# Kernel tuning notes

Hardware: AMD Instinct MI355X
Metric: run time of the kernel (lower is better)

## Reference

```python
import jax, jax.numpy as jnp
import numpy as np

U1, U2, FEAT = 24, 48, 16
LN_EPS = 1e-3  # tf.keras LayerNormalization default


def _ln(x, gamma, beta):
    mu = jnp.mean(x, axis=-1, keepdims=True)
    var = jnp.mean(jnp.square(x - mu), axis=-1, keepdims=True)
    return (x - mu) * jax.lax.rsqrt(var + LN_EPS) * gamma + beta


def setup_inputs() -> dict:
    key = jax.random.key(0)
    ks = jax.random.split(key, 8)
    B, T = 8192, 256
    sequence = jax.random.normal(ks[0], (B, T, FEAT), dtype=jnp.float32)
    s = 0.1
    return {
        "sequence": sequence,
        "W1": jax.random.normal(ks[1], (FEAT, U1), dtype=jnp.float32) * s,
        "b1": jnp.zeros((U1,), jnp.float32),
        "Wr1": jax.random.normal(ks[2], (U1, U1), dtype=jnp.float32) * s,
        "br1": jnp.zeros((U1,), jnp.float32),
        "g1": jnp.ones((U1,), jnp.float32),
        "be1": jnp.zeros((U1,), jnp.float32),
        "W2": jax.random.normal(ks[3], (U1, U2), dtype=jnp.float32) * s,
        "b2": jnp.zeros((U2,), jnp.float32),
        "Wr2": jax.random.normal(ks[4], (U2, U2), dtype=jnp.float32) * s,
        "br2": jnp.zeros((U2,), jnp.float32),
        "g2": jnp.ones((U2,), jnp.float32),
        "be2": jnp.zeros((U2,), jnp.float32),
        "Wout": jax.random.normal(ks[5], (U2, 1), dtype=jnp.float32) * s,
        "bout": jnp.zeros((1,), jnp.float32),
    }


def reference(sequence, W1, b1, Wr1, br1, g1, be1, W2, b2, Wr2, br2, g2, be2, Wout, bout):
    B = sequence.shape[0]
    xs = jnp.swapaxes(sequence, 0, 1)  # [T, B, F]

    def step(carry, inp):
        s1, s2 = carry
        x = inp @ W1 + b1 + s1
        ns1 = jnp.tanh(x @ Wr1 + br1)
        h = _ln(ns1, g1, be1)
        y = h @ W2 + b2 + s2
        ns2 = jnp.tanh(y @ Wr2 + br2)
        return (ns1, ns2), None

    init = (jnp.zeros((B, U1), sequence.dtype), jnp.zeros((B, U2), sequence.dtype))
    (s1, s2), _ = jax.lax.scan(step, init, xs)
    last_out = _ln(s2, g2, be2)  # output of final timestep (return_sequences=False)
    return jax.nn.sigmoid(last_out @ Wout + bout)  # [B, 1]
```

## Files before the change

kernel.cpp:

```cpp
#include <hip/hip_runtime.h>

#define T_STEPS 256
#define FEAT 16
#define U1 24
#define U2 48
#define SLOTS 8

typedef short bf16x8 __attribute__((ext_vector_type(8)));
typedef float f32x4 __attribute__((ext_vector_type(4)));

__device__ __forceinline__ unsigned short f2bf(float f) {
    unsigned u = __float_as_uint(f);
    u += 0x7fffu + ((u >> 16) & 1u);
    return (unsigned short)(u >> 16);
}

#if defined(__has_builtin)
#if __has_builtin(__builtin_amdgcn_cvt_pk_bf16_f32)
#define HAVE_PKBF16 1
#endif
#if __has_builtin(__builtin_amdgcn_rcpf)
#define HAVE_RCP 1
#endif
#if __has_builtin(__builtin_amdgcn_rsqf)
#define HAVE_RSQ 1
#endif
#if __has_builtin(__builtin_amdgcn_exp2f)
#define HAVE_EXP2 1
#endif
#endif

__device__ __forceinline__ unsigned pk2(float a, float b) {
#ifdef HAVE_PKBF16
    typedef __bf16 bf2 __attribute__((ext_vector_type(2)));
    union { bf2 v; unsigned u; } cv;
    cv.v = __builtin_amdgcn_cvt_pk_bf16_f32(a, b);
    return cv.u;
#else
    return (unsigned)f2bf(a) | ((unsigned)f2bf(b) << 16);
#endif
}
__device__ __forceinline__ float bfr(float x) {
    return __uint_as_float(((unsigned)f2bf(x)) << 16);
}

__device__ __forceinline__ float hrcp(float x) {
#ifdef HAVE_RCP
    return __builtin_amdgcn_rcpf(x);
#else
    return 1.0f / x;
#endif
}
__device__ __forceinline__ float hrsq(float x) {
#ifdef HAVE_RSQ
    return __builtin_amdgcn_rsqf(x);
#else
    return rsqrtf(x);
#endif
}
__device__ __forceinline__ float hexp2(float x) {
#ifdef HAVE_EXP2
    return __builtin_amdgcn_exp2f(x);
#else
    return exp2f(x);
#endif
}
__device__ __forceinline__ float fast_tanh(float z) {
    const float e = hexp2(z * 2.8853900817779268f);
    return fmaf(-2.0f, hrcp(1.0f + e), 1.0f);
}

union FragU { bf16x8 v; unsigned u[4]; };

#define MFMA(A, B, C) __builtin_amdgcn_mfma_f32_16x16x32_bf16((A), (B), (C), 0, 0, 0)

__device__ __forceinline__ void bar_sync() {
    asm volatile("" ::: "memory");
    __builtin_amdgcn_s_waitcnt(0xC07F);
    __builtin_amdgcn_s_barrier();
    asm volatile("" ::: "memory");
}


__global__ __launch_bounds__(128) void rnn_kernel(
    const float* __restrict__ seq,
    const float* __restrict__ W1, const float* __restrict__ b1,
    const float* __restrict__ Wr1, const float* __restrict__ br1,
    const float* __restrict__ g1, const float* __restrict__ be1,
    const float* __restrict__ W2, const float* __restrict__ b2,
    const float* __restrict__ Wr2, const float* __restrict__ br2,
    const float* __restrict__ g2, const float* __restrict__ be2,
    const float* __restrict__ Wout, const float* __restrict__ bout,
    float* __restrict__ out)
{
    __shared__ __align__(16) unsigned ringN[SLOTS][64][4];
    __shared__ __align__(16) unsigned ringQ[SLOTS][64][4];

    const int tid = threadIdx.x;
    const int w = tid >> 6;
    const int lane = tid & 63;
    const int j15 = lane & 15;
    const int g = lane >> 4;
    const f32x4 z4 = {0.f, 0.f, 0.f, 0.f};

    if (w == 0) {
        bf16x8 A1[2], A2[2];
#pragma unroll
        for (int t = 0; t < 2; ++t) {
            const int m = 16 * t + j15;
            FragU f1, f2;
#pragma unroll
            for (int j = 0; j < 8; ++j) {
                const int k = 8 * g + j;
                const int u = (j < 4) ? 4 * g + j : 16 + 4 * g + (j - 4);
                float v1 = 0.f, v2 = 0.f;
                if (m < U1) {
                    if (k < FEAT) v1 = W1[k * U1 + m];
                    else if (k == FEAT) v1 = b1[m];
                    if (u < U1) v2 = Wr1[u * U1 + m];
                    else if (u == U1) v2 = br1[m];
                } else if (m == U1 && k == FEAT) {
                    v1 = 1.f;
                }
                f1.v[j] = (short)f2bf(v1);
                f2.v[j] = (short)f2bf(v2);
            }
            A1[t] = f1.v; A2[t] = f2.v;
        }
        const unsigned cdw0 = (g == 2) ? 0x00003F80u : 0u;

        const float* sp = seq + (size_t)(blockIdx.x * 16 + j15) * (T_STEPS * FEAT) + 8 * g;
        const bool ld = (lane < 32);

        f32x4 s1[2] = {z4, z4};

        auto pstep = [&](int t, const float4 ca, const float4 cb) {
            FragU inf;
            const unsigned p0 = pk2(ca.x, ca.y), p1 = pk2(ca.z, ca.w);
            const unsigned p2 = pk2(cb.x, cb.y), p3 = pk2(cb.z, cb.w);
            const bool lo = (g < 2);
            inf.u[0] = lo ? p0 : cdw0;
            inf.u[1] = lo ? p1 : 0u;
            inf.u[2] = lo ? p2 : 0u;
            inf.u[3] = lo ? p3 : 0u;

            const f32x4 x0 = MFMA(A1[0], inf.v, s1[0]);
            const f32x4 x1 = MFMA(A1[1], inf.v, s1[1]);

            FragU xf;
            xf.u[0] = pk2(x0[0], x0[1]); xf.u[1] = pk2(x0[2], x0[3]);
            xf.u[2] = pk2(x1[0], x1[1]); xf.u[3] = pk2(x1[2], x1[3]);

            const f32x4 d0 = MFMA(A2[0], xf.v, z4);
            const f32x4 d1 = MFMA(A2[1], xf.v, z4);
            float n1a[4], n1b[4], qa[4], qb[4];
#pragma unroll
            for (int r = 0; r < 4; ++r) {
                n1a[r] = fast_tanh(d0[r]); n1b[r] = fast_tanh(d1[r]);
                qa[r] = n1a[r] * n1a[r];   qb[r] = n1b[r] * n1b[r];
                s1[0][r] = n1a[r];         s1[1][r] = n1b[r];
            }
            FragU nf, qf;
            nf.u[0] = pk2(n1a[0], n1a[1]); nf.u[1] = pk2(n1a[2], n1a[3]);
            nf.u[2] = pk2(n1b[0], n1b[1]); nf.u[3] = pk2(n1b[2], n1b[3]);
            qf.u[0] = pk2(qa[0], qa[1]);   qf.u[1] = pk2(qa[2], qa[3]);
            qf.u[2] = pk2(qb[0], qb[1]);   qf.u[3] = pk2(qb[2], qb[3]);
            const int slot = t & (SLOTS - 1);
            *(uint4*)&ringN[slot][lane][0] = make_uint4(nf.u[0], nf.u[1], nf.u[2], nf.u[3]);
            *(uint4*)&ringQ[slot][lane][0] = make_uint4(qf.u[0], qf.u[1], qf.u[2], qf.u[3]);
        };

        float4 ca[4], cb[4], na[4], nb[4];
        if (ld) {
#pragma unroll
            for (int i = 0; i < 4; ++i) {
                ca[i] = *(const float4*)(sp + i * 16);
                cb[i] = *(const float4*)(sp + i * 16 + 4);
            }
        }
#pragma unroll 1
        for (int j = 0; j < 64; ++j) {
            const int jn = (j + 1 < 64) ? j + 1 : j;
            if (ld) {
#pragma unroll
                for (int i = 0; i < 4; ++i) {
                    na[i] = *(const float4*)(sp + (4 * jn + i) * 16);
                    nb[i] = *(const float4*)(sp + (4 * jn + i) * 16 + 4);
                }
            }
#pragma unroll
            for (int i = 0; i < 4; ++i) pstep(4 * j + i, ca[i], cb[i]);
            bar_sync();
#pragma unroll
            for (int i = 0; i < 4; ++i) { ca[i] = na[i]; cb[i] = nb[i]; }
        }
        bar_sync();
    } else {
        bf16x8 A3a[4], A3b3, A4[3][2];
#pragma unroll
        for (int t = 0; t < 3; ++t) {
            const int m = 16 * t + j15;
            FragU f3, f4a, f4b;
#pragma unroll
            for (int j = 0; j < 8; ++j) {
                const int u = (j < 4) ? 4 * g + j : 16 + 4 * g + (j - 4);
                f3.v[j] = (short)f2bf(u < U1 ? g1[u] * W2[u * U2 + m] : 0.f);
                f4a.v[j] = (short)f2bf(Wr2[u * U2 + m]);
                float vb = 0.f;
                if (j < 4) vb = Wr2[(32 + 4 * g + j) * U2 + m];
                else if (j == 4 && g == 0) vb = br2[m];
                f4b.v[j] = (short)f2bf(vb);
            }
            A3a[t] = f3.v; A4[t][0] = f4a.v; A4[t][1] = f4b.v;
        }
        {
            FragU fa, fb;
#pragma unroll
            for (int j = 0; j < 8; ++j) {
                const int u = (j < 4) ? 4 * g + j : 16 + 4 * g + (j - 4);
                fa.v[j] = ((j15 & 3) == 0 && u < U1) ? (short)0x3F80 : (short)0;
                fb.v[j] = ((j15 & 3) == 1 && u < U1) ? (short)0x3F80 : (short)0;
            }
            A3a[3] = fa.v; A3b3 = fb.v;
        }
        float cC[12], dC[12];
#pragma unroll
        for (int i = 0; i < 12; ++i) {
            const int m = 16 * (i >> 2) + 4 * g + (i & 3);
            float cc = 0.f, dd = b2[m];
            for (int k = 0; k < U1; ++k) {
                const float wq = bfr(g1[k] * W2[k * U2 + m]);
                cc += wq;
                dd += be1[k] * W2[k * U2 + m];
            }
            cC[i] = cc; dC[i] = dd;
        }
        f32x4 s2[3] = {z4, z4, z4};

        auto cstep = [&](int t) {
            const int slot = t & (SLOTS - 1);
            const bf16x8 hf0 = *(const bf16x8*)&ringN[slot][lane][0];
            const bf16x8 hf1 = *(const bf16x8*)&ringQ[slot][lane][0];

            f32x4 sAcc = MFMA(A3a[3], hf0, z4);
            sAcc = MFMA(A3b3, hf1, sAcc);
            const f32x4 P0 = MFMA(A3a[0], hf0, z4);
            const f32x4 P1 = MFMA(A3a[1], hf0, z4);
            const f32x4 P2 = MFMA(A3a[2], hf0, z4);

            const float mu = sAcc[0] * (1.f / U1);
            const float var = sAcc[1] * (1.f / U1) - mu * mu;
            const float rs = hrsq(var + 1e-3f);

            float y[12];
#pragma unroll
            for (int r = 0; r < 4; ++r) {
                y[r]     = fmaf(rs, fmaf(-mu, cC[r],     P0[r]), dC[r]     + s2[0][r]);
                y[4 + r] = fmaf(rs, fmaf(-mu, cC[4 + r], P1[r]), dC[4 + r] + s2[1][r]);
                y[8 + r] = fmaf(rs, fmaf(-mu, cC[8 + r], P2[r]), dC[8 + r] + s2[2][r]);
            }

            FragU yf0, yf1;
            yf0.u[0] = pk2(y[0], y[1]);  yf0.u[1] = pk2(y[2], y[3]);
            yf0.u[2] = pk2(y[4], y[5]);  yf0.u[3] = pk2(y[6], y[7]);
            yf1.u[0] = pk2(y[8], y[9]);  yf1.u[1] = pk2(y[10], y[11]);
            yf1.u[2] = (g == 0) ? 0x00003F80u : 0u;
            yf1.u[3] = 0u;

#pragma unroll
            for (int t3 = 0; t3 < 3; ++t3) {
                f32x4 e = MFMA(A4[t3][0], yf0.v, z4);
                e = MFMA(A4[t3][1], yf1.v, e);
#pragma unroll
                for (int r = 0; r < 4; ++r) s2[t3][r] = fast_tanh(e[r]);
            }
        };

        bar_sync();
#pragma unroll 1
        for (int j = 0; j < 64; ++j) {
#pragma unroll
            for (int i = 0; i < 4; ++i) cstep(4 * j + i);
            bar_sync();
        }

        float g2r[12], be2r[12], wor[12];
#pragma unroll
        for (int r = 0; r < 12; ++r) {
            const int n = 16 * (r >> 2) + 4 * g + (r & 3);
            g2r[r] = g2[n]; be2r[r] = be2[n]; wor[r] = Wout[n];
        }
        float sm = 0.f, sq = 0.f;
#pragma unroll
        for (int tt = 0; tt < 3; ++tt)
#pragma unroll
            for (int r = 0; r < 4; ++r) { const float v = s2[tt][r]; sm += v; sq += v * v; }
        sm += __shfl_xor(sm, 16, 64); sq += __shfl_xor(sq, 16, 64);
        sm += __shfl_xor(sm, 32, 64); sq += __shfl_xor(sq, 32, 64);
        const float mu = sm * (1.f / U2);
        const float var = sq * (1.f / U2) - mu * mu;
        const float rs = hrsq(var + 1e-3f);
        float p = 0.f;
#pragma unroll
        for (int tt = 0; tt < 3; ++tt)
#pragma unroll
            for (int r = 0; r < 4; ++r)
                p += ((s2[tt][r] - mu) * rs * g2r[4 * tt + r] + be2r[4 * tt + r]) * wor[4 * tt + r];
        p += __shfl_xor(p, 16, 64);
        p += __shfl_xor(p, 32, 64);
        if (lane < 16) {
            const float z = p + bout[0];
            const float e = hexp2(-z * 1.4426950408889634f);
            out[blockIdx.x * 16 + lane] = hrcp(1.0f + e);
        }
    }
}

extern "C" void kernel_launch(void* const* d_in, const int* in_sizes, int n_in,
                              void* d_out, int out_size, void* d_ws, size_t ws_size,
                              hipStream_t stream) {
    const float* seq  = (const float*)d_in[0];
    const float* W1   = (const float*)d_in[1];
    const float* b1   = (const float*)d_in[2];
    const float* Wr1  = (const float*)d_in[3];
    const float* br1  = (const float*)d_in[4];
    const float* g1   = (const float*)d_in[5];
    const float* be1  = (const float*)d_in[6];
    const float* W2   = (const float*)d_in[7];
    const float* b2   = (const float*)d_in[8];
    const float* Wr2  = (const float*)d_in[9];
    const float* br2  = (const float*)d_in[10];
    const float* g2   = (const float*)d_in[11];
    const float* be2  = (const float*)d_in[12];
    const float* Wout = (const float*)d_in[13];
    const float* bout = (const float*)d_in[14];
    float* out = (float*)d_out;

    const int B = in_sizes[0] / (T_STEPS * FEAT);
    const int grid = B / 16;
    rnn_kernel<<<grid, 128, 0, stream>>>(seq, W1, b1, Wr1, br1, g1, be1,
                                         W2, b2, Wr2, br2, g2, be2, Wout, bout, out);
}
```

Measured before the change: 286.8 us.

## Move LayerNorm sum reductions to producer wave and split dependent MFMA chains

The producer wave now computes the per-row sum and sum-of-squares of the layer-1 state with two extra MFMAs and writes only those scalars to a small LDS ring, instead of writing the full squared-activation fragment. The consumer wave no longer reads the squared fragment or runs its two dependent reduction MFMAs, which shortens its critical path. It also issues the two layer-2 recurrent MFMAs independently and adds the results, rather than chaining the accumulator. The cost is extra MFMA work and a second LDS store on the producer wave.

```diff
diff --git a/kernel.cpp b/kernel.cpp
--- a/kernel.cpp
+++ b/kernel.cpp
@@ -94,7 +94,7 @@
     float* __restrict__ out)
 {
     __shared__ __align__(16) unsigned ringN[SLOTS][64][4];
-    __shared__ __align__(16) unsigned ringQ[SLOTS][64][4];
+    __shared__ __align__(8)  float    ringS[SLOTS][16][2];
 
     const int tid = threadIdx.x;
     const int w = tid >> 6;
@@ -104,7 +104,7 @@
     const f32x4 z4 = {0.f, 0.f, 0.f, 0.f};
 
     if (w == 0) {
-        bf16x8 A1[2], A2[2];
+        bf16x8 A1[2], A2[2], Asum;
 #pragma unroll
         for (int t = 0; t < 2; ++t) {
             const int m = 16 * t + j15;
@@ -127,6 +127,15 @@
             }
             A1[t] = f1.v; A2[t] = f2.v;
         }
+        {
+            FragU fs;
+#pragma unroll
+            for (int j = 0; j < 8; ++j) {
+                const int u = (j < 4) ? 4 * g + j : 16 + 4 * g + (j - 4);
+                fs.v[j] = (j15 == 0 && u < U1) ? (short)0x3F80 : (short)0;
+            }
+            Asum = fs.v;
+        }
         const unsigned cdw0 = (g == 2) ? 0x00003F80u : 0u;
 
         const float* sp = seq + (size_t)(blockIdx.x * 16 + j15) * (T_STEPS * FEAT) + 8 * g;
@@ -165,9 +174,13 @@
             nf.u[2] = pk2(n1b[0], n1b[1]); nf.u[3] = pk2(n1b[2], n1b[3]);
             qf.u[0] = pk2(qa[0], qa[1]);   qf.u[1] = pk2(qa[2], qa[3]);
             qf.u[2] = pk2(qb[0], qb[1]);   qf.u[3] = pk2(qb[2], qb[3]);
+
+            const f32x4 sA = MFMA(Asum, nf.v, z4);
+            const f32x4 sB = MFMA(Asum, qf.v, z4);
+
             const int slot = t & (SLOTS - 1);
             *(uint4*)&ringN[slot][lane][0] = make_uint4(nf.u[0], nf.u[1], nf.u[2], nf.u[3]);
-            *(uint4*)&ringQ[slot][lane][0] = make_uint4(qf.u[0], qf.u[1], qf.u[2], qf.u[3]);
+            if (g == 0) *(float2*)&ringS[slot][j15][0] = make_float2(sA[0], sB[0]);
         };
 
         float4 ca[4], cb[4], na[4], nb[4];
@@ -196,7 +209,7 @@
         }
         bar_sync();
     } else {
-        bf16x8 A3a[4], A3b3, A4[3][2];
+        bf16x8 A3[3], A4[3][2];
 #pragma unroll
         for (int t = 0; t < 3; ++t) {
             const int m = 16 * t + j15;
@@ -211,17 +224,7 @@
                 else if (j == 4 && g == 0) vb = br2[m];
                 f4b.v[j] = (short)f2bf(vb);
             }
-            A3a[t] = f3.v; A4[t][0] = f4a.v; A4[t][1] = f4b.v;
-        }
-        {
-            FragU fa, fb;
-#pragma unroll
-            for (int j = 0; j < 8; ++j) {
-                const int u = (j < 4) ? 4 * g + j : 16 + 4 * g + (j - 4);
-                fa.v[j] = ((j15 & 3) == 0 && u < U1) ? (short)0x3F80 : (short)0;
-                fb.v[j] = ((j15 & 3) == 1 && u < U1) ? (short)0x3F80 : (short)0;
-            }
-            A3a[3] = fa.v; A3b3 = fb.v;
+            A3[t] = f3.v; A4[t][0] = f4a.v; A4[t][1] = f4b.v;
         }
         float cC[12], dC[12];
 #pragma unroll
@@ -240,17 +243,15 @@
         auto cstep = [&](int t) {
             const int slot = t & (SLOTS - 1);
             const bf16x8 hf0 = *(const bf16x8*)&ringN[slot][lane][0];
-            const bf16x8 hf1 = *(const bf16x8*)&ringQ[slot][lane][0];
-
-            f32x4 sAcc = MFMA(A3a[3], hf0, z4);
-            sAcc = MFMA(A3b3, hf1, sAcc);
-            const f32x4 P0 = MFMA(A3a[0], hf0, z4);
-            const f32x4 P1 = MFMA(A3a[1], hf0, z4);
-            const f32x4 P2 = MFMA(A3a[2], hf0, z4);
-
-            const float mu = sAcc[0] * (1.f / U1);
-            const float var = sAcc[1] * (1.f / U1) - mu * mu;
+            const float2 ss = *(const float2*)&ringS[slot][j15][0];
+
+            const float mu = ss.x * (1.f / U1);
+            const float var = ss.y * (1.f / U1) - mu * mu;
             const float rs = hrsq(var + 1e-3f);
+
+            const f32x4 P0 = MFMA(A3[0], hf0, z4);
+            const f32x4 P1 = MFMA(A3[1], hf0, z4);
+            const f32x4 P2 = MFMA(A3[2], hf0, z4);
 
             float y[12];
 #pragma unroll
@@ -269,10 +270,10 @@
 
 #pragma unroll
             for (int t3 = 0; t3 < 3; ++t3) {
-                f32x4 e = MFMA(A4[t3][0], yf0.v, z4);
-                e = MFMA(A4[t3][1], yf1.v, e);
-#pragma unroll
-                for (int r = 0; r < 4; ++r) s2[t3][r] = fast_tanh(e[r]);
+                const f32x4 e1 = MFMA(A4[t3][0], yf0.v, z4);
+                const f32x4 e2 = MFMA(A4[t3][1], yf1.v, z4);
+#pragma unroll
+                for (int r = 0; r < 4; ++r) s2[t3][r] = fast_tanh(e1[r] + e2[r]);
             }
         };
 
```

New measurement: 374.8 us. 1.31x slower.
